# Performance work log

Hardware: AMD Instinct MI355X
Metric: run time of the kernel (lower is better)

The kernel has to match this reference:

```python
import jax, jax.numpy as jnp
import numpy as np
import math

B, H, N, D = 4, 8, 2048, 64


def setup_inputs() -> dict:
    key = jax.random.key(0)
    kq, kk, kv = jax.random.split(key, 3)
    q = jax.random.normal(kq, (B, H, N, D), dtype=jnp.float32)
    k = jax.random.normal(kk, (B, H, N, D), dtype=jnp.float32)
    v = jax.random.normal(kv, (B, H, N, D), dtype=jnp.float32)
    return {"q": q, "k": k, "v": v}


def reference(q, k, v):
    # global_attention_Sub: expanded squared L2 distance ||q_i - k_j||^2
    # = qq_i - 2 q_i.k_j + kk_j, then softmax(-dist/sqrt(D)) @ v.
    scale = math.sqrt(q.shape[-1])
    inner = -2.0 * jnp.einsum('bhnd,bhmd->bhnm', q, k)          # [B,H,N,N]
    qq = jnp.sum(q * q, axis=-1, keepdims=True)                  # [B,H,N,1]
    kk = jnp.sum(k * k, axis=-1, keepdims=True)                  # [B,H,N,1]
    diff_sq = qq + inner + jnp.swapaxes(kk, -1, -2)              # [B,H,N,N]
    attn = jax.nn.softmax(-diff_sq / scale, axis=-1)
    x = jnp.einsum('bhnm,bhmd->bhnd', attn, v)                   # [B,H,N,D]
    return jnp.transpose(x, (0, 2, 1, 3))                        # [B,N,H,D]
```

## Files before the change

kernel.cpp:

```cpp
#include <hip/hip_runtime.h>

typedef __bf16 bf16x8 __attribute__((ext_vector_type(8)));
typedef float floatx4 __attribute__((ext_vector_type(4)));
typedef float floatx16 __attribute__((ext_vector_type(16)));
typedef unsigned int uintx4 __attribute__((ext_vector_type(4)));

constexpr int Bc = 4, Hc = 8, Nc = 2048, Dc = 64;
constexpr int BQ = 128;
constexpr int WQ = 32;
constexpr int TK = 64;
constexpr int NT = Nc / TK;
constexpr int NT2 = NT / 2;
constexpr float LOG2E = 1.44269504088896340736f;

constexpr size_t KSW_OFF = 0;
constexpr size_t VSW_OFF = (size_t)32 * NT * 8192;
constexpr size_t KKN_OFF = VSW_OFF * 2;

constexpr int SK_OFF = 0;
constexpr int SV_OFF = 32768;
constexpr int SL_OFF = 65536;
constexpr int EXCH_OFF = 0;
constexpr int SMEM_BYTES = 65536 + 1024;

typedef __attribute__((address_space(1))) const unsigned int gu32;
typedef __attribute__((address_space(3))) unsigned int lu32;
__device__ __forceinline__ void dma16(const void* g, void* l) {
    __builtin_amdgcn_global_load_lds((gu32*)g, (lu32*)l, 16, 0, 0);
}

__device__ __forceinline__ unsigned pk2(float lo, float hi) {
    unsigned short a = __builtin_bit_cast(unsigned short, (__bf16)lo);
    unsigned short b = __builtin_bit_cast(unsigned short, (__bf16)hi);
    return (unsigned)a | ((unsigned)b << 16);
}

__global__ __launch_bounds__(256) void prep_kernel(
    const float* __restrict__ Kg, const float* __restrict__ Vg, char* __restrict__ ws)
{
    __shared__ float sT[64 * 68];
    const int tid = threadIdx.x;
    const int jt = blockIdx.x, bh = blockIdx.y;

    __bf16* Ksw = (__bf16*)(ws + KSW_OFF) + ((size_t)bh * NT + jt) * 4096;
    __bf16* Vsw = (__bf16*)(ws + VSW_OFF) + ((size_t)bh * NT + jt) * 4096;
    float*  kkn = (float*)(ws + KKN_OFF) + (size_t)bh * Nc + jt * 64;
    const size_t tb = ((size_t)bh * Nc + jt * 64) * Dc;

#pragma unroll
    for (int cc = 0; cc < 2; ++cc) {
        const int g   = tid + cc * 256;
        const int key = g >> 3, kcx = g & 7;
        const int kc  = kcx ^ (key & 7);
        const float* src = Kg + tb + key * 64 + kc * 8;
        float4 a = *(const float4*)src;
        float4 b = *(const float4*)(src + 4);
        float ss = a.x*a.x + a.y*a.y + a.z*a.z + a.w*a.w
                 + b.x*b.x + b.y*b.y + b.z*b.z + b.w*b.w;
        ss += __shfl_xor(ss, 1);
        ss += __shfl_xor(ss, 2);
        ss += __shfl_xor(ss, 4);
        if (kcx == 0) {
            const int k5 = key & 31, kt = key >> 5;
            const int rlo = k5 & 3, hh = (k5 >> 2) & 1, rhi = k5 >> 3;
            kkn[kt * 32 + hh * 16 + rhi * 4 + rlo] = -(ss * 0.125f * LOG2E);
        }
        bf16x8 c8;
        c8[0]=(__bf16)a.x; c8[1]=(__bf16)a.y; c8[2]=(__bf16)a.z; c8[3]=(__bf16)a.w;
        c8[4]=(__bf16)b.x; c8[5]=(__bf16)b.y; c8[6]=(__bf16)b.z; c8[7]=(__bf16)b.w;
        *(bf16x8*)(Ksw + g * 8) = c8;
    }
    {
        const int js = tid >> 2, dc = (tid & 3) * 16;
        const float* vr = Vg + tb + js * 64 + dc;
        float* dst = &sT[js * 68 + dc];
        *(float4*)dst       = *(const float4*)vr;
        *(float4*)(dst + 4) = *(const float4*)(vr + 4);
        *(float4*)(dst + 8) = *(const float4*)(vr + 8);
        *(float4*)(dst + 12)= *(const float4*)(vr + 12);
    }
    __syncthreads();
#pragma unroll
    for (int cc = 0; cc < 2; ++cc) {
        const int g = tid + cc * 256;
        const int d = g >> 3, kcx = g & 7;
        const int kc = kcx ^ (d & 7);
        bf16x8 c8;
#pragma unroll
        for (int e = 0; e < 8; ++e) {
            const int ee = (e + kcx) & 7;
            c8[ee] = (__bf16)sT[(kc * 8 + ee) * 68 + d];
        }
        *(bf16x8*)(Vsw + g * 8) = c8;
    }
}

__global__ __launch_bounds__(512, 4) void attn_kernel(
    const float* __restrict__ Qg, const char* __restrict__ ws, float* __restrict__ Og)
{
    __shared__ __align__(16) char smem[SMEM_BYTES];

    const int tid  = threadIdx.x;
    const int wave = tid >> 6;
    const int grp  = wave >> 2;
    const int sw   = wave & 3;
    const int lane = tid & 63;
    const int r31  = lane & 31;
    const int hi   = lane >> 5;

    const int qt = blockIdx.x;
    const int bh = blockIdx.y;

    const char* Kimg = ws + KSW_OFF + (size_t)bh * NT * 8192;
    const char* Vimg = ws + VSW_OFF + (size_t)bh * NT * 8192;
    const float* kkp = (const float*)(ws + KKN_OFF) + (size_t)bh * Nc;

    const float qscale = 0.25f * LOG2E;
    const int i0 = qt * BQ + sw * WQ;

    bf16x8 qf[4];
    {
        const float* qrow = Qg + ((size_t)bh * Nc + i0 + r31) * Dc + hi * 8;
#pragma unroll
        for (int ks = 0; ks < 4; ++ks) {
            float4 a = *(const float4*)(qrow + ks * 16);
            float4 b = *(const float4*)(qrow + ks * 16 + 4);
            bf16x8 f;
            f[0] = (__bf16)(a.x * qscale); f[1] = (__bf16)(a.y * qscale);
            f[2] = (__bf16)(a.z * qscale); f[3] = (__bf16)(a.w * qscale);
            f[4] = (__bf16)(b.x * qscale); f[5] = (__bf16)(b.y * qscale);
            f[6] = (__bf16)(b.z * qscale); f[7] = (__bf16)(b.w * qscale);
            qf[ks] = f;
        }
    }

    int off4[4];
#pragma unroll
    for (int ks = 0; ks < 4; ++ks)
        off4[ks] = r31 * 128 + (((ks * 2 + hi) ^ (r31 & 7)) << 4);

    floatx16 oacc[2];
#pragma unroll
    for (int dt = 0; dt < 2; ++dt)
#pragma unroll
        for (int e = 0; e < 16; ++e) oacc[dt][e] = 0.f;
    float lpr = 0.f;

    auto stage = [&](int t2, int nb) {
        const size_t tb = (size_t)(2 * t2) * 8192;
        const int off = tid * 16;
        dma16(Kimg + tb + off,        smem + SK_OFF + nb * 8192 + off);
        dma16(Kimg + tb + 8192 + off, smem + SK_OFF + 16384 + nb * 8192 + off);
        dma16(Vimg + tb + off,        smem + SV_OFF + nb * 8192 + off);
        dma16(Vimg + tb + 8192 + off, smem + SV_OFF + 16384 + nb * 8192 + off);
    };

    stage(0, 0);

    for (int t = 0; t < NT2; ++t) {
        const int b = t & 1;
        __syncthreads();
        if (t + 1 < NT2) stage(t + 1, b ^ 1);

        const int jt = 2 * t + grp;
        const char* kb = smem + SK_OFF + grp * 16384 + b * 8192;
        const char* vb = smem + SV_OFF + grp * 16384 + b * 8192;

        floatx16 st[2];
        const float* kkb = kkp + jt * 64 + hi * 16;
#pragma unroll
        for (int kt = 0; kt < 2; ++kt) {
#pragma unroll
            for (int gi = 0; gi < 4; ++gi) {
                floatx4 kv = *(const floatx4*)(kkb + kt * 32 + gi * 4);
                st[kt][gi * 4 + 0] = kv[0]; st[kt][gi * 4 + 1] = kv[1];
                st[kt][gi * 4 + 2] = kv[2]; st[kt][gi * 4 + 3] = kv[3];
            }
        }

#pragma unroll
        for (int kt = 0; kt < 2; ++kt)
#pragma unroll
            for (int ks = 0; ks < 4; ++ks) {
                bf16x8 kf = *(const bf16x8*)(kb + kt * 4096 + off4[ks]);
                st[kt] = __builtin_amdgcn_mfma_f32_32x32x16_bf16(kf, qf[ks], st[kt], 0, 0, 0);
            }

#pragma unroll
        for (int kt = 0; kt < 2; ++kt) {
            float p[16];
#pragma unroll
            for (int r = 0; r < 16; ++r) {
                p[r] = __builtin_amdgcn_exp2f(st[kt][r]);
                lpr += p[r];
            }
            unsigned w[4][2];
#pragma unroll
            for (int g = 0; g < 4; ++g) {
                w[g][0] = pk2(p[4 * g + 0], p[4 * g + 1]);
                w[g][1] = pk2(p[4 * g + 2], p[4 * g + 3]);
            }
#pragma unroll
            for (int sub = 0; sub < 2; ++sub) {
                unsigned a0 = w[2 * sub][0],     a1 = w[2 * sub][1];
                unsigned b0 = w[2 * sub + 1][0], b1 = w[2 * sub + 1][1];
                asm("v_permlane32_swap_b32 %0, %1" : "+v"(a0), "+v"(b0));
                asm("v_permlane32_swap_b32 %0, %1" : "+v"(a1), "+v"(b1));
                uintx4 u; u[0] = a0; u[1] = a1; u[2] = b0; u[3] = b1;
                bf16x8 pa = __builtin_bit_cast(bf16x8, u);
                const int ks = kt * 2 + sub;
#pragma unroll
                for (int dt = 0; dt < 2; ++dt) {
                    bf16x8 vf = *(const bf16x8*)(vb + dt * 4096 + off4[ks]);
                    oacc[dt] = __builtin_amdgcn_mfma_f32_32x32x16_bf16(pa, vf, oacc[dt], 0, 0, 0);
                }
            }
        }
    }

    {
        float l = lpr + __shfl_xor(lpr, 32);
        if (!hi) *(float*)(smem + SL_OFF + (grp * 128 + sw * 32 + r31) * 4) = l;
    }
    __syncthreads();

    {
        char* slot = smem + EXCH_OFF + wave * 4096;
        if (grp == 0) {
#pragma unroll
            for (int r = 0; r < 16; ++r)
                *(float*)(slot + r * 256 + lane * 4) = oacc[1][r];
        } else {
#pragma unroll
            for (int r = 0; r < 16; ++r)
                *(float*)(slot + r * 256 + lane * 4) = oacc[0][r];
        }
    }
    __syncthreads();

    floatx16 osum;
    if (grp == 0) osum = oacc[0]; else osum = oacc[1];
    {
        const char* slot = smem + EXCH_OFF + (wave ^ 4) * 4096;
#pragma unroll
        for (int r = 0; r < 16; ++r)
            osum[r] += *(const float*)(slot + r * 256 + lane * 4);
    }

    const float* slp = (const float*)(smem + SL_OFF);
    const int b_ = bh >> 3, hh = bh & 7;
#pragma unroll
    for (int g = 0; g < 4; ++g) {
        floatx4 la = *(const floatx4*)(slp + sw * 32 + 8 * g + 4 * hi);
        floatx4 lb = *(const floatx4*)(slp + 128 + sw * 32 + 8 * g + 4 * hi);
#pragma unroll
        for (int rlo = 0; rlo < 4; ++rlo) {
            const float inv = 1.f / (la[rlo] + lb[rlo]);
            const int i = i0 + 8 * g + 4 * hi + rlo;
            float* orow = Og + (((size_t)b_ * Nc + i) * Hc + hh) * Dc + grp * 32 + r31;
            orow[0] = osum[4 * g + rlo] * inv;
        }
    }
}

extern "C" void kernel_launch(void* const* d_in, const int* in_sizes, int n_in,
                              void* d_out, int out_size, void* d_ws, size_t ws_size,
                              hipStream_t stream) {
    const float* q = (const float*)d_in[0];
    const float* k = (const float*)d_in[1];
    const float* v = (const float*)d_in[2];
    float* out = (float*)d_out;
    char* ws = (char*)d_ws;
    prep_kernel<<<dim3(NT, Bc * Hc), 256, 0, stream>>>(k, v, ws);
    attn_kernel<<<dim3(Nc / BQ, Bc * Hc), 512, 0, stream>>>(q, ws, out);
}
```

Before: 140.1 us.

## Give each wave two 32-row query groups to reuse K/V fragments

Halves the block to 256 threads (4 waves), and each wave now handles 64 query rows as two 32-row groups. Each K and V fragment read from LDS feeds two MFMAs, which halves LDS read traffic per unit of compute. The staging loop, the cross-group exchange and the final normalization are reworked to match. In exchange, each wave holds more registers for accumulators and Q fragments, and the block has fewer waves to hide latency and DMA.

```diff
diff --git a/kernel.cpp b/kernel.cpp
--- a/kernel.cpp
+++ b/kernel.cpp
@@ -7,7 +7,7 @@
 
 constexpr int Bc = 4, Hc = 8, Nc = 2048, Dc = 64;
 constexpr int BQ = 128;
-constexpr int WQ = 32;
+constexpr int WQ = 64;
 constexpr int TK = 64;
 constexpr int NT = Nc / TK;
 constexpr int NT2 = NT / 2;
@@ -20,7 +20,6 @@
 constexpr int SK_OFF = 0;
 constexpr int SV_OFF = 32768;
 constexpr int SL_OFF = 65536;
-constexpr int EXCH_OFF = 0;
 constexpr int SMEM_BYTES = 65536 + 1024;
 
 typedef __attribute__((address_space(1))) const unsigned int gu32;
@@ -95,15 +94,15 @@
     }
 }
 
-__global__ __launch_bounds__(512, 4) void attn_kernel(
+__global__ __launch_bounds__(256, 2) void attn_kernel(
     const float* __restrict__ Qg, const char* __restrict__ ws, float* __restrict__ Og)
 {
     __shared__ __align__(16) char smem[SMEM_BYTES];
 
     const int tid  = threadIdx.x;
     const int wave = tid >> 6;
-    const int grp  = wave >> 2;
-    const int sw   = wave & 3;
+    const int grp  = wave >> 1;
+    const int sw   = wave & 1;
     const int lane = tid & 63;
     const int r31  = lane & 31;
     const int hi   = lane >> 5;
@@ -118,9 +117,10 @@
     const float qscale = 0.25f * LOG2E;
     const int i0 = qt * BQ + sw * WQ;
 
-    bf16x8 qf[4];
-    {
-        const float* qrow = Qg + ((size_t)bh * Nc + i0 + r31) * Dc + hi * 8;
+    bf16x8 qf[2][4];
+#pragma unroll
+    for (int qg = 0; qg < 2; ++qg) {
+        const float* qrow = Qg + ((size_t)bh * Nc + i0 + qg * 32 + r31) * Dc + hi * 8;
 #pragma unroll
         for (int ks = 0; ks < 4; ++ks) {
             float4 a = *(const float4*)(qrow + ks * 16);
@@ -130,7 +130,7 @@
             f[2] = (__bf16)(a.z * qscale); f[3] = (__bf16)(a.w * qscale);
             f[4] = (__bf16)(b.x * qscale); f[5] = (__bf16)(b.y * qscale);
             f[6] = (__bf16)(b.z * qscale); f[7] = (__bf16)(b.w * qscale);
-            qf[ks] = f;
+            qf[qg][ks] = f;
         }
     }
 
@@ -139,20 +139,26 @@
     for (int ks = 0; ks < 4; ++ks)
         off4[ks] = r31 * 128 + (((ks * 2 + hi) ^ (r31 & 7)) << 4);
 
-    floatx16 oacc[2];
-#pragma unroll
-    for (int dt = 0; dt < 2; ++dt)
-#pragma unroll
-        for (int e = 0; e < 16; ++e) oacc[dt][e] = 0.f;
-    float lpr = 0.f;
-
-    auto stage = [&](int t2, int nb) {
-        const size_t tb = (size_t)(2 * t2) * 8192;
+    floatx16 oacc[2][2];
+#pragma unroll
+    for (int qg = 0; qg < 2; ++qg)
+#pragma unroll
+        for (int dt = 0; dt < 2; ++dt)
+#pragma unroll
+            for (int e = 0; e < 16; ++e) oacc[qg][dt][e] = 0.f;
+    float lpr[2] = {0.f, 0.f};
+
+    auto stage = [&](int t, int nb) {
+        const size_t tb = (size_t)t * 16384;
         const int off = tid * 16;
-        dma16(Kimg + tb + off,        smem + SK_OFF + nb * 8192 + off);
-        dma16(Kimg + tb + 8192 + off, smem + SK_OFF + 16384 + nb * 8192 + off);
-        dma16(Vimg + tb + off,        smem + SV_OFF + nb * 8192 + off);
-        dma16(Vimg + tb + 8192 + off, smem + SV_OFF + 16384 + nb * 8192 + off);
+#pragma unroll
+        for (int i = 0; i < 4; ++i)
+            dma16(Kimg + tb + i * 4096 + off,
+                  smem + SK_OFF + (i >> 1) * 16384 + nb * 8192 + (i & 1) * 4096 + off);
+#pragma unroll
+        for (int i = 0; i < 4; ++i)
+            dma16(Vimg + tb + i * 4096 + off,
+                  smem + SV_OFF + (i >> 1) * 16384 + nb * 8192 + (i & 1) * 4096 + off);
     };
 
     stage(0, 0);
@@ -165,100 +171,107 @@
         const int jt = 2 * t + grp;
         const char* kb = smem + SK_OFF + grp * 16384 + b * 8192;
         const char* vb = smem + SV_OFF + grp * 16384 + b * 8192;
-
-        floatx16 st[2];
         const float* kkb = kkp + jt * 64 + hi * 16;
+
 #pragma unroll
         for (int kt = 0; kt < 2; ++kt) {
+            floatx16 st0;
 #pragma unroll
             for (int gi = 0; gi < 4; ++gi) {
                 floatx4 kv = *(const floatx4*)(kkb + kt * 32 + gi * 4);
-                st[kt][gi * 4 + 0] = kv[0]; st[kt][gi * 4 + 1] = kv[1];
-                st[kt][gi * 4 + 2] = kv[2]; st[kt][gi * 4 + 3] = kv[3];
+                st0[gi * 4 + 0] = kv[0]; st0[gi * 4 + 1] = kv[1];
+                st0[gi * 4 + 2] = kv[2]; st0[gi * 4 + 3] = kv[3];
             }
-        }
-
-#pragma unroll
-        for (int kt = 0; kt < 2; ++kt)
+            floatx16 st1 = st0;
+
 #pragma unroll
             for (int ks = 0; ks < 4; ++ks) {
                 bf16x8 kf = *(const bf16x8*)(kb + kt * 4096 + off4[ks]);
-                st[kt] = __builtin_amdgcn_mfma_f32_32x32x16_bf16(kf, qf[ks], st[kt], 0, 0, 0);
+                st0 = __builtin_amdgcn_mfma_f32_32x32x16_bf16(kf, qf[0][ks], st0, 0, 0, 0);
+                st1 = __builtin_amdgcn_mfma_f32_32x32x16_bf16(kf, qf[1][ks], st1, 0, 0, 0);
             }
 
-#pragma unroll
-        for (int kt = 0; kt < 2; ++kt) {
-            float p[16];
-#pragma unroll
-            for (int r = 0; r < 16; ++r) {
-                p[r] = __builtin_amdgcn_exp2f(st[kt][r]);
-                lpr += p[r];
+            bf16x8 pa[2][2];
+#pragma unroll
+            for (int qg = 0; qg < 2; ++qg) {
+                const floatx16& stq = qg ? st1 : st0;
+                float p[16];
+#pragma unroll
+                for (int r = 0; r < 16; ++r) {
+                    p[r] = __builtin_amdgcn_exp2f(stq[r]);
+                    lpr[qg] += p[r];
+                }
+                unsigned w[4][2];
+#pragma unroll
+                for (int g = 0; g < 4; ++g) {
+                    w[g][0] = pk2(p[4 * g + 0], p[4 * g + 1]);
+                    w[g][1] = pk2(p[4 * g + 2], p[4 * g + 3]);
+                }
+#pragma unroll
+                for (int sub = 0; sub < 2; ++sub) {
+                    unsigned a0 = w[2 * sub][0],     a1 = w[2 * sub][1];
+                    unsigned b0 = w[2 * sub + 1][0], b1 = w[2 * sub + 1][1];
+                    asm("v_permlane32_swap_b32 %0, %1" : "+v"(a0), "+v"(b0));
+                    asm("v_permlane32_swap_b32 %0, %1" : "+v"(a1), "+v"(b1));
+                    uintx4 u; u[0] = a0; u[1] = a1; u[2] = b0; u[3] = b1;
+                    pa[qg][sub] = __builtin_bit_cast(bf16x8, u);
+                }
             }
-            unsigned w[4][2];
-#pragma unroll
-            for (int g = 0; g < 4; ++g) {
-                w[g][0] = pk2(p[4 * g + 0], p[4 * g + 1]);
-                w[g][1] = pk2(p[4 * g + 2], p[4 * g + 3]);
-            }
-#pragma unroll
-            for (int sub = 0; sub < 2; ++sub) {
-                unsigned a0 = w[2 * sub][0],     a1 = w[2 * sub][1];
-                unsigned b0 = w[2 * sub + 1][0], b1 = w[2 * sub + 1][1];
-                asm("v_permlane32_swap_b32 %0, %1" : "+v"(a0), "+v"(b0));
-                asm("v_permlane32_swap_b32 %0, %1" : "+v"(a1), "+v"(b1));
-                uintx4 u; u[0] = a0; u[1] = a1; u[2] = b0; u[3] = b1;
-                bf16x8 pa = __builtin_bit_cast(bf16x8, u);
-                const int ks = kt * 2 + sub;
+
+#pragma unroll
+            for (int sub = 0; sub < 2; ++sub)
 #pragma unroll
                 for (int dt = 0; dt < 2; ++dt) {
-                    bf16x8 vf = *(const bf16x8*)(vb + dt * 4096 + off4[ks]);
-                    oacc[dt] = __builtin_amdgcn_mfma_f32_32x32x16_bf16(pa, vf, oacc[dt], 0, 0, 0);
-                }
-            }
-        }
-    }
+                    bf16x8 vf = *(const bf16x8*)(vb + dt * 4096 + off4[kt * 2 + sub]);
+                    oacc[0][dt] = __builtin_amdgcn_mfma_f32_32x32x16_bf16(pa[0][sub], vf, oacc[0][dt], 0, 0, 0);
+                    oacc[1][dt] = __builtin_amdgcn_mfma_f32_32x32x16_bf16(pa[1][sub], vf, oacc[1][dt], 0, 0, 0);
+                }
+        }
+    }
+
+#pragma unroll
+    for (int qg = 0; qg < 2; ++qg) {
+        float l = lpr[qg] + __shfl_xor(lpr[qg], 32);
+        if (!hi) *(float*)(smem + SL_OFF + (grp * 128 + sw * 64 + qg * 32 + r31) * 4) = l;
+    }
+    __syncthreads();
 
     {
-        float l = lpr + __shfl_xor(lpr, 32);
-        if (!hi) *(float*)(smem + SL_OFF + (grp * 128 + sw * 32 + r31) * 4) = l;
+        char* slot = smem + wave * 8192;
+#pragma unroll
+        for (int qg = 0; qg < 2; ++qg)
+#pragma unroll
+            for (int r = 0; r < 16; ++r)
+                *(float*)(slot + (qg * 16 + r) * 256 + lane * 4) = oacc[qg][grp ^ 1][r];
     }
     __syncthreads();
 
+    floatx16 osum[2];
+#pragma unroll
+    for (int qg = 0; qg < 2; ++qg) osum[qg] = oacc[qg][grp];
     {
-        char* slot = smem + EXCH_OFF + wave * 4096;
-        if (grp == 0) {
+        const char* pslot = smem + (wave ^ 2) * 8192;
+#pragma unroll
+        for (int qg = 0; qg < 2; ++qg)
 #pragma unroll
             for (int r = 0; r < 16; ++r)
-                *(float*)(slot + r * 256 + lane * 4) = oacc[1][r];
-        } else {
-#pragma unroll
-            for (int r = 0; r < 16; ++r)
-                *(float*)(slot + r * 256 + lane * 4) = oacc[0][r];
-        }
-    }
-    __syncthreads();
-
-    floatx16 osum;
-    if (grp == 0) osum = oacc[0]; else osum = oacc[1];
-    {
-        const char* slot = smem + EXCH_OFF + (wave ^ 4) * 4096;
-#pragma unroll
-        for (int r = 0; r < 16; ++r)
-            osum[r] += *(const float*)(slot + r * 256 + lane * 4);
+                osum[qg][r] += *(const float*)(pslot + (qg * 16 + r) * 256 + lane * 4);
     }
 
     const float* slp = (const float*)(smem + SL_OFF);
     const int b_ = bh >> 3, hh = bh & 7;
 #pragma unroll
+    for (int qg = 0; qg < 2; ++qg)
+#pragma unroll
     for (int g = 0; g < 4; ++g) {
-        floatx4 la = *(const floatx4*)(slp + sw * 32 + 8 * g + 4 * hi);
-        floatx4 lb = *(const floatx4*)(slp + 128 + sw * 32 + 8 * g + 4 * hi);
+        floatx4 la = *(const floatx4*)(slp + sw * 64 + qg * 32 + 8 * g + 4 * hi);
+        floatx4 lb = *(const floatx4*)(slp + 128 + sw * 64 + qg * 32 + 8 * g + 4 * hi);
 #pragma unroll
         for (int rlo = 0; rlo < 4; ++rlo) {
             const float inv = 1.f / (la[rlo] + lb[rlo]);
-            const int i = i0 + 8 * g + 4 * hi + rlo;
+            const int i = i0 + qg * 32 + 8 * g + 4 * hi + rlo;
             float* orow = Og + (((size_t)b_ * Nc + i) * Hc + hh) * Dc + grp * 32 + r31;
-            orow[0] = osum[4 * g + rlo] * inv;
+            orow[0] = osum[qg][4 * g + rlo] * inv;
         }
     }
 }
@@ -272,5 +285,5 @@
     float* out = (float*)d_out;
     char* ws = (char*)d_ws;
     prep_kernel<<<dim3(NT, Bc * Hc), 256, 0, stream>>>(k, v, ws);
-    attn_kernel<<<dim3(Nc / BQ, Bc * Hc), 512, 0, stream>>>(q, ws, out);
-}
+    attn_kernel<<<dim3(Nc / BQ, Bc * Hc), 256, 0, stream>>>(q, ws, out);
+}
```

Measured after the change: 203.4 us. +45.2%, slower.

## Load V fragments directly from global into registers, halving LDS footprint

Applied to the files above, without the earlier changes.

V tiles are no longer staged through LDS by DMA. Each lane now reads its V MFMA fragments straight from a re-laid-out global V image (prep kernel writes V in fragment order without swizzle), which halves shared memory use and could raise occupancy. The K prefetch is moved after the kk loads, the PV MFMAs are batched after the exp/pack step, and s_setprio brackets the MFMA bursts. The trade-off is that redundant per-wave global/L2 reads of V replace shared LDS reuse, which adds latency that is not explicitly double-buffered.

```diff
diff --git a/kernel.cpp b/kernel.cpp
--- a/kernel.cpp
+++ b/kernel.cpp
@@ -18,10 +18,8 @@
 constexpr size_t KKN_OFF = VSW_OFF * 2;
 
 constexpr int SK_OFF = 0;
-constexpr int SV_OFF = 32768;
-constexpr int SL_OFF = 65536;
-constexpr int EXCH_OFF = 0;
-constexpr int SMEM_BYTES = 65536 + 1024;
+constexpr int SL_OFF = 32768;
+constexpr int SMEM_BYTES = 32768 + 1024;
 
 typedef __attribute__((address_space(1))) const unsigned int gu32;
 typedef __attribute__((address_space(3))) unsigned int lu32;
@@ -83,14 +81,13 @@
 #pragma unroll
     for (int cc = 0; cc < 2; ++cc) {
         const int g = tid + cc * 256;
-        const int d = g >> 3, kcx = g & 7;
-        const int kc = kcx ^ (d & 7);
+        const int r31o = g & 31, hio = (g >> 5) & 1, kso = (g >> 6) & 3, dto = g >> 8;
+        const int d  = dto * 32 + r31o;
+        const int kc = kso * 2 + hio;
         bf16x8 c8;
 #pragma unroll
-        for (int e = 0; e < 8; ++e) {
-            const int ee = (e + kcx) & 7;
-            c8[ee] = (__bf16)sT[(kc * 8 + ee) * 68 + d];
-        }
+        for (int e = 0; e < 8; ++e)
+            c8[e] = (__bf16)sT[(kc * 8 + e) * 68 + d];
         *(bf16x8*)(Vsw + g * 8) = c8;
     }
 }
@@ -146,25 +143,20 @@
         for (int e = 0; e < 16; ++e) oacc[dt][e] = 0.f;
     float lpr = 0.f;
 
-    auto stage = [&](int t2, int nb) {
-        const size_t tb = (size_t)(2 * t2) * 8192;
+    auto stageK = [&](int t, int nb) {
+        const size_t tb = (size_t)t * 16384;
         const int off = tid * 16;
         dma16(Kimg + tb + off,        smem + SK_OFF + nb * 8192 + off);
         dma16(Kimg + tb + 8192 + off, smem + SK_OFF + 16384 + nb * 8192 + off);
-        dma16(Vimg + tb + off,        smem + SV_OFF + nb * 8192 + off);
-        dma16(Vimg + tb + 8192 + off, smem + SV_OFF + 16384 + nb * 8192 + off);
     };
 
-    stage(0, 0);
+    stageK(0, 0);
 
     for (int t = 0; t < NT2; ++t) {
         const int b = t & 1;
         __syncthreads();
-        if (t + 1 < NT2) stage(t + 1, b ^ 1);
 
         const int jt = 2 * t + grp;
-        const char* kb = smem + SK_OFF + grp * 16384 + b * 8192;
-        const char* vb = smem + SV_OFF + grp * 16384 + b * 8192;
 
         floatx16 st[2];
         const float* kkb = kkp + jt * 64 + hi * 16;
@@ -178,6 +170,20 @@
             }
         }
 
+        if (t + 1 < NT2) stageK(t + 1, b ^ 1);
+
+        bf16x8 vfr[2][4];
+        {
+            const char* vsrc = Vimg + (size_t)jt * 8192 + lane * 16;
+#pragma unroll
+            for (int dt = 0; dt < 2; ++dt)
+#pragma unroll
+                for (int kc = 0; kc < 4; ++kc)
+                    vfr[dt][kc] = *(const bf16x8*)(vsrc + dt * 4096 + kc * 1024);
+        }
+
+        const char* kb = smem + SK_OFF + grp * 16384 + b * 8192;
+        __builtin_amdgcn_s_setprio(1);
 #pragma unroll
         for (int kt = 0; kt < 2; ++kt)
 #pragma unroll
@@ -185,7 +191,9 @@
                 bf16x8 kf = *(const bf16x8*)(kb + kt * 4096 + off4[ks]);
                 st[kt] = __builtin_amdgcn_mfma_f32_32x32x16_bf16(kf, qf[ks], st[kt], 0, 0, 0);
             }
-
+        __builtin_amdgcn_s_setprio(0);
+
+        bf16x8 pa[2][2];
 #pragma unroll
         for (int kt = 0; kt < 2; ++kt) {
             float p[16];
@@ -207,15 +215,20 @@
                 asm("v_permlane32_swap_b32 %0, %1" : "+v"(a0), "+v"(b0));
                 asm("v_permlane32_swap_b32 %0, %1" : "+v"(a1), "+v"(b1));
                 uintx4 u; u[0] = a0; u[1] = a1; u[2] = b0; u[3] = b1;
-                bf16x8 pa = __builtin_bit_cast(bf16x8, u);
-                const int ks = kt * 2 + sub;
-#pragma unroll
-                for (int dt = 0; dt < 2; ++dt) {
-                    bf16x8 vf = *(const bf16x8*)(vb + dt * 4096 + off4[ks]);
-                    oacc[dt] = __builtin_amdgcn_mfma_f32_32x32x16_bf16(pa, vf, oacc[dt], 0, 0, 0);
-                }
-            }
-        }
+                pa[kt][sub] = __builtin_bit_cast(bf16x8, u);
+            }
+        }
+
+        __builtin_amdgcn_s_setprio(1);
+#pragma unroll
+        for (int kt = 0; kt < 2; ++kt)
+#pragma unroll
+            for (int sub = 0; sub < 2; ++sub)
+#pragma unroll
+                for (int dt = 0; dt < 2; ++dt)
+                    oacc[dt] = __builtin_amdgcn_mfma_f32_32x32x16_bf16(
+                        pa[kt][sub], vfr[dt][kt * 2 + sub], oacc[dt], 0, 0, 0);
+        __builtin_amdgcn_s_setprio(0);
     }
 
     {
@@ -225,7 +238,7 @@
     __syncthreads();
 
     {
-        char* slot = smem + EXCH_OFF + wave * 4096;
+        char* slot = smem + wave * 4096;
         if (grp == 0) {
 #pragma unroll
             for (int r = 0; r < 16; ++r)
@@ -241,10 +254,10 @@
     floatx16 osum;
     if (grp == 0) osum = oacc[0]; else osum = oacc[1];
     {
-        const char* slot = smem + EXCH_OFF + (wave ^ 4) * 4096;
+        const char* pslot = smem + (wave ^ 4) * 4096;
 #pragma unroll
         for (int r = 0; r < 16; ++r)
-            osum[r] += *(const float*)(slot + r * 256 + lane * 4);
+            osum[r] += *(const float*)(pslot + r * 256 + lane * 4);
     }
 
     const float* slp = (const float*)(smem + SL_OFF);
```

Result: slower. 160.0 us (+14.2%).

## Remap blocks to XCDs, start QK MFMA from zero, add wave priorities

Applied to the files above, without the earlier changes.

Block indices are remapped so that all query tiles of one (batch, head) land on the same XCD, which is meant to improve L2 reuse of the K/V images. The QK^T MFMA chain now starts from a zero accumulator and the kk bias is added just before exp2, so the bias loads are no longer on the MFMA dependency path. s_setprio raises wave priority around the MFMA sections to interleave matrix and exp work across waves. The remap assumes grid dimensions of 16x32 and 8 XCDs.

```diff
diff --git a/kernel.cpp b/kernel.cpp
--- a/kernel.cpp
+++ b/kernel.cpp
@@ -20,7 +20,6 @@
 constexpr int SK_OFF = 0;
 constexpr int SV_OFF = 32768;
 constexpr int SL_OFF = 65536;
-constexpr int EXCH_OFF = 0;
 constexpr int SMEM_BYTES = 65536 + 1024;
 
 typedef __attribute__((address_space(1))) const unsigned int gu32;
@@ -108,8 +107,10 @@
     const int r31  = lane & 31;
     const int hi   = lane >> 5;
 
-    const int qt = blockIdx.x;
-    const int bh = blockIdx.y;
+    const int lin  = blockIdx.x + (blockIdx.y << 4);
+    const int xcd  = lin & 7, slot = lin >> 3;
+    const int bh   = (xcd << 2) | (slot >> 4);
+    const int qt   = slot & 15;
 
     const char* Kimg = ws + KSW_OFF + (size_t)bh * NT * 8192;
     const char* Vimg = ws + VSW_OFF + (size_t)bh * NT * 8192;
@@ -146,8 +147,12 @@
         for (int e = 0; e < 16; ++e) oacc[dt][e] = 0.f;
     float lpr = 0.f;
 
-    auto stage = [&](int t2, int nb) {
-        const size_t tb = (size_t)(2 * t2) * 8192;
+    floatx16 zacc;
+#pragma unroll
+    for (int e = 0; e < 16; ++e) zacc[e] = 0.f;
+
+    auto stage = [&](int t, int nb) {
+        const size_t tb = (size_t)t * 16384;
         const int off = tid * 16;
         dma16(Kimg + tb + off,        smem + SK_OFF + nb * 8192 + off);
         dma16(Kimg + tb + 8192 + off, smem + SK_OFF + 16384 + nb * 8192 + off);
@@ -166,32 +171,37 @@
         const char* kb = smem + SK_OFF + grp * 16384 + b * 8192;
         const char* vb = smem + SV_OFF + grp * 16384 + b * 8192;
 
-        floatx16 st[2];
+        floatx16 kkv[2];
         const float* kkb = kkp + jt * 64 + hi * 16;
 #pragma unroll
-        for (int kt = 0; kt < 2; ++kt) {
+        for (int kt = 0; kt < 2; ++kt)
 #pragma unroll
             for (int gi = 0; gi < 4; ++gi) {
                 floatx4 kv = *(const floatx4*)(kkb + kt * 32 + gi * 4);
-                st[kt][gi * 4 + 0] = kv[0]; st[kt][gi * 4 + 1] = kv[1];
-                st[kt][gi * 4 + 2] = kv[2]; st[kt][gi * 4 + 3] = kv[3];
-            }
-        }
-
-#pragma unroll
-        for (int kt = 0; kt < 2; ++kt)
-#pragma unroll
-            for (int ks = 0; ks < 4; ++ks) {
+                kkv[kt][gi * 4 + 0] = kv[0]; kkv[kt][gi * 4 + 1] = kv[1];
+                kkv[kt][gi * 4 + 2] = kv[2]; kkv[kt][gi * 4 + 3] = kv[3];
+            }
+
+        floatx16 st[2];
+        __builtin_amdgcn_s_setprio(1);
+#pragma unroll
+        for (int kt = 0; kt < 2; ++kt) {
+            bf16x8 kf0 = *(const bf16x8*)(kb + kt * 4096 + off4[0]);
+            st[kt] = __builtin_amdgcn_mfma_f32_32x32x16_bf16(kf0, qf[0], zacc, 0, 0, 0);
+#pragma unroll
+            for (int ks = 1; ks < 4; ++ks) {
                 bf16x8 kf = *(const bf16x8*)(kb + kt * 4096 + off4[ks]);
                 st[kt] = __builtin_amdgcn_mfma_f32_32x32x16_bf16(kf, qf[ks], st[kt], 0, 0, 0);
             }
+        }
+        __builtin_amdgcn_s_setprio(0);
 
 #pragma unroll
         for (int kt = 0; kt < 2; ++kt) {
             float p[16];
 #pragma unroll
             for (int r = 0; r < 16; ++r) {
-                p[r] = __builtin_amdgcn_exp2f(st[kt][r]);
+                p[r] = __builtin_amdgcn_exp2f(st[kt][r] + kkv[kt][r]);
                 lpr += p[r];
             }
             unsigned w[4][2];
@@ -200,6 +210,7 @@
                 w[g][0] = pk2(p[4 * g + 0], p[4 * g + 1]);
                 w[g][1] = pk2(p[4 * g + 2], p[4 * g + 3]);
             }
+            __builtin_amdgcn_s_setprio(1);
 #pragma unroll
             for (int sub = 0; sub < 2; ++sub) {
                 unsigned a0 = w[2 * sub][0],     a1 = w[2 * sub][1];
@@ -215,6 +226,7 @@
                     oacc[dt] = __builtin_amdgcn_mfma_f32_32x32x16_bf16(pa, vf, oacc[dt], 0, 0, 0);
                 }
             }
+            __builtin_amdgcn_s_setprio(0);
         }
     }
 
@@ -225,7 +237,7 @@
     __syncthreads();
 
     {
-        char* slot = smem + EXCH_OFF + wave * 4096;
+        char* slot = smem + wave * 4096;
         if (grp == 0) {
 #pragma unroll
             for (int r = 0; r < 16; ++r)
@@ -241,10 +253,10 @@
     floatx16 osum;
     if (grp == 0) osum = oacc[0]; else osum = oacc[1];
     {
-        const char* slot = smem + EXCH_OFF + (wave ^ 4) * 4096;
+        const char* pslot = smem + (wave ^ 4) * 4096;
 #pragma unroll
         for (int r = 0; r < 16; ++r)
-            osum[r] += *(const float*)(slot + r * 256 + lane * 4);
+            osum[r] += *(const float*)(pslot + r * 256 + lane * 4);
     }
 
     const float* slp = (const float*)(smem + SL_OFF);
```

New measurement: 149.6 us. 1.07x slower.
